# Performance work log

Measured on AMD Instinct MI355X. Metric: run time of the kernel, lower is better.

Reference implementation:

```python
import jax, jax.numpy as jnp
import numpy as np

B, T, TR, DIM, H = 1, 4096, 1024, 1536, 12
DH = DIM // H          # 128
EPS = 1e-6             # RMSNorm eps
REF_SCALE = 1.0


def setup_inputs() -> dict:
    key = jax.random.key(0)
    ks = jax.random.split(key, 20)
    s = 0.02
    w = lambda k: jax.random.normal(k, (DIM, DIM), jnp.float32) * s
    b = lambda k: jax.random.normal(k, (DIM,), jnp.float32) * 0.01
    theta = jax.random.uniform(ks[2], (T, DH // 2), jnp.float32) * (2.0 * np.pi)
    return {
        "hidden_states": jax.random.normal(ks[0], (B, T, DIM), jnp.float32),
        "ref_hidden_states": jax.random.normal(ks[1], (B, TR, DIM), jnp.float32),
        "rot_cos": jnp.cos(theta),
        "rot_sin": jnp.sin(theta),
        "Wq": w(ks[3]), "bq": b(ks[4]),
        "Wk": w(ks[5]), "bk": b(ks[6]),
        "Wv": w(ks[7]), "bv": b(ks[8]),
        "Wkr": w(ks[9]), "bkr": b(ks[10]),
        "Wvr": w(ks[11]), "bvr": b(ks[12]),
        "Wo": w(ks[13]), "bo": b(ks[14]),
        "gq": jnp.ones((DIM,), jnp.float32),
        "gk": jnp.ones((DIM,), jnp.float32),
    }


def _rmsnorm(x, g):
    return x * jax.lax.rsqrt(jnp.mean(x * x, axis=-1, keepdims=True) + EPS) * g


def _heads(x):  # [B, T, DIM] -> [B, H, T, DH]
    return x.reshape(B, -1, H, DH).transpose(0, 2, 1, 3)


def _merge(x):  # [B, H, T, DH] -> [B, T, DIM]
    return x.transpose(0, 2, 1, 3).reshape(B, -1, DIM)


def _rope(x, c, s):
    # consecutive pairs along DH form complex numbers (view_as_complex semantics)
    xe, xo = x[..., 0::2], x[..., 1::2]
    c = c[None, None]  # [1,1,T,DH/2]
    s = s[None, None]
    re = xe * c - xo * s
    im = xe * s + xo * c
    return jnp.stack([re, im], axis=-1).reshape(x.shape)


def _attn(q, k, v):
    scale = 1.0 / jnp.sqrt(jnp.asarray(DH, q.dtype))
    p = jax.nn.softmax(jnp.einsum("bhqd,bhkd->bhqk", q, k) * scale, axis=-1)
    return jnp.einsum("bhqk,bhkd->bhqd", p, v)


def reference(hidden_states, ref_hidden_states, rot_cos, rot_sin,
              Wq, bq, Wk, bk, Wv, bv, Wkr, bkr, Wvr, bvr, Wo, bo, gq, gk):
    # QKV projections (self-attention: encoder_hidden_states = hidden_states)
    q_lin = hidden_states @ Wq + bq
    k_lin = hidden_states @ Wk + bk
    v_lin = hidden_states @ Wv + bv

    # ---- reference-attention branch (uses pre-RoPE query) ----
    ref_q = _heads(_rmsnorm(q_lin, gq))
    ref_k = _heads(_rmsnorm(ref_hidden_states @ Wkr + bkr, gk))
    ref_v = _heads(ref_hidden_states @ Wvr + bvr)
    ref_out = _merge(_attn(ref_q, ref_k, ref_v))  # [B, T, DIM]

    # ---- main attention with QK-norm + RoPE ----
    q = _rope(_heads(_rmsnorm(q_lin, gq)), rot_cos, rot_sin)
    k = _rope(_heads(_rmsnorm(k_lin, gk)), rot_cos, rot_sin)
    v = _heads(v_lin)
    main_out = _merge(_attn(q, k, v))  # [B, T, DIM]

    # scaled residual combine + output projection (dropout = identity)
    out = main_out + REF_SCALE * ref_out
    return out @ Wo + bo
```

## Files before the change

### kernel.cpp

```cpp
#include <hip/hip_runtime.h>

typedef unsigned short u16;
typedef unsigned int u32;
typedef __attribute__((ext_vector_type(8))) short short8;
typedef __attribute__((ext_vector_type(4))) float f32x4;

__device__ inline u16 f2b(float f) {
  u32 u = __builtin_bit_cast(u32, f);
  u += 0x7fff + ((u >> 16) & 1);
  return (u16)(u >> 16);
}
__device__ inline float b2f(u16 u) {
  return __builtin_bit_cast(float, (u32)u << 16);
}
__device__ inline u32 pack_bf16_rn(float a, float b) {
  const u32 ua = __builtin_bit_cast(u32, a) + 0x8000u;
  const u32 ub = __builtin_bit_cast(u32, b) + 0x8000u;
  return (ua >> 16) | (ub & 0xffff0000u);
}
__device__ inline void c_store(float* p, float v) { *p = v; }
__device__ inline void c_store(u16* p, float v) { *p = f2b(v); }

__device__ inline float fexp2(float x) {
#if __has_builtin(__builtin_amdgcn_exp2f)
  return __builtin_amdgcn_exp2f(x);
#else
  return exp2f(x);
#endif
}

typedef const __attribute__((address_space(1))) u32 gu32;
typedef __attribute__((address_space(3))) u32 lu32;
__device__ inline void async16(const u16* g, u16* l) {
  __builtin_amdgcn_global_load_lds((gu32*)g, (lu32*)l, 16, 0, 0);
}

#define QS (0.08838834764831843f * 1.4426950408889634f)

template <int MI, typename TC>
__global__ __launch_bounds__(256) void gemm128_kernel(
    const u16* __restrict__ A, long lda,
    const u16* __restrict__ Bt, long ldb,
    TC* __restrict__ C0, TC* __restrict__ C1, TC* __restrict__ C2, long ldc,
    const float* b0, const float* b1, const float* b2,
    int K) {
  __shared__ u16 As[32 * MI * 32];
  __shared__ u16 Bs[128 * 32];

  const int tid = threadIdx.x;
  const int lane = tid & 63;
  const int w = tid >> 6;
  const int r = lane & 15;
  const int quad = lane >> 4;
  const int m0 = blockIdx.y * (32 * MI);
  const int nb = blockIdx.x * 128;
  const int seg = nb / 1536;
  const int nc = nb - seg * 1536;
  TC* C = seg == 0 ? C0 : (seg == 1 ? C1 : C2);
  const float* bias = seg == 0 ? b0 : (seg == 1 ? b1 : b2);

  const int srow = lane >> 2;
  const int sx = ((lane & 3) ^ (srow & 3)) * 8;
  const u16* Ag = A + (size_t)(m0 + w * 8 * MI + srow) * lda + sx;
  const u16* Bg = Bt + (size_t)(nb + w * 32 + srow) * ldb + sx;
  u16* Al[MI / 2];
#pragma unroll
  for (int j = 0; j < MI / 2; ++j) Al[j] = &As[(w * 8 * MI + 16 * j) * 32];
  u16* const Bl0 = &Bs[(w * 32) * 32];
  u16* const Bl1 = &Bs[(w * 32 + 16) * 32];

  const int wm = (w >> 1) * (16 * MI);
  const int wn = (w & 1) * 64;

  f32x4 acc[MI][4];
#pragma unroll
  for (int i = 0; i < MI; ++i)
#pragma unroll
    for (int j = 0; j < 4; ++j) acc[i][j] = (f32x4){0.f, 0.f, 0.f, 0.f};

  const int fco = (quad ^ (r & 3)) * 8;

  for (int kk = 0; kk < K; kk += 32) {
    __syncthreads();
#pragma unroll
    for (int j = 0; j < MI / 2; ++j) async16(Ag + kk + (size_t)(16 * j) * lda, Al[j]);
    async16(Bg + kk, Bl0);
    async16(Bg + kk + 16 * ldb, Bl1);
    __syncthreads();

    short8 af[MI], bf[4];
#pragma unroll
    for (int mi = 0; mi < MI; ++mi)
      af[mi] = *reinterpret_cast<const short8*>(&As[(wm + 16 * mi + r) * 32 + fco]);
#pragma unroll
    for (int ni = 0; ni < 4; ++ni)
      bf[ni] = *reinterpret_cast<const short8*>(&Bs[(wn + 16 * ni + r) * 32 + fco]);
#pragma unroll
    for (int mi = 0; mi < MI; ++mi)
#pragma unroll
      for (int ni = 0; ni < 4; ++ni)
        acc[mi][ni] = __builtin_amdgcn_mfma_f32_16x16x32_bf16(af[mi], bf[ni], acc[mi][ni], 0, 0, 0);
  }

#pragma unroll
  for (int mi = 0; mi < MI; ++mi)
#pragma unroll
    for (int ni = 0; ni < 4; ++ni)
#pragma unroll
      for (int rr = 0; rr < 4; ++rr) {
        const int row = m0 + wm + 16 * mi + 4 * quad + rr;
        const int col = nc + wn + 16 * ni + r;
        c_store(&C[(size_t)row * ldc + col], acc[mi][ni][rr] + bias[col]);
      }
}

__global__ __launch_bounds__(256) void conv2_kernel(
    const float* __restrict__ xa, u16* __restrict__ ya, int n8a,
    const float* __restrict__ xb, u16* __restrict__ yb, int n8b) {
  int i = blockIdx.x * 256 + threadIdx.x;
  const float* x;
  u16* y;
  if (i < n8a) {
    x = xa; y = ya;
  } else {
    i -= n8a;
    if (i >= n8b) return;
    x = xb; y = yb;
  }
  const float4 v0 = reinterpret_cast<const float4*>(x)[2 * i];
  const float4 v1 = reinterpret_cast<const float4*>(x)[2 * i + 1];
  uint4 rv;
  rv.x = (u32)f2b(v0.x) | ((u32)f2b(v0.y) << 16);
  rv.y = (u32)f2b(v0.z) | ((u32)f2b(v0.w) << 16);
  rv.z = (u32)f2b(v1.x) | ((u32)f2b(v1.y) << 16);
  rv.w = (u32)f2b(v1.z) | ((u32)f2b(v1.w) << 16);
  reinterpret_cast<uint4*>(y)[i] = rv;
}

__device__ inline void transconv_body(const float* __restrict__ W, u16* __restrict__ Wt) {
  __shared__ u16 Ls[64 * 72];
  const int tid = threadIdx.x;
  const int k0 = blockIdx.y * 64;
  const int n0 = blockIdx.x * 64;
#pragma unroll
  for (int i = 0; i < 4; ++i) {
    const int c = tid + 256 * i;
    const int row = c >> 4;
    const int c4 = (c & 15) * 4;
    const float4 v = *reinterpret_cast<const float4*>(&W[(size_t)(k0 + row) * 1536 + n0 + c4]);
    Ls[(c4 + 0) * 72 + row] = f2b(v.x);
    Ls[(c4 + 1) * 72 + row] = f2b(v.y);
    Ls[(c4 + 2) * 72 + row] = f2b(v.z);
    Ls[(c4 + 3) * 72 + row] = f2b(v.w);
  }
  __syncthreads();
#pragma unroll
  for (int i = 0; i < 2; ++i) {
    const int c = tid + 256 * i;
    const int n = c >> 3;
    const int kc = (c & 7) * 8;
    u16 tmp[8];
#pragma unroll
    for (int j = 0; j < 8; ++j) tmp[j] = Ls[n * 72 + kc + j];
    *reinterpret_cast<uint4*>(&Wt[(size_t)(n0 + n) * 1536 + k0 + kc]) =
        *reinterpret_cast<const uint4*>(tmp);
  }
}

__global__ __launch_bounds__(256) void transconv6_kernel(
    const float* W0, const float* W1, const float* W2,
    const float* W3, const float* W4, const float* W5,
    u16* T0, u16* T1, u16* T2, u16* T3, u16* T4, u16* T5) {
  const int z = blockIdx.z;
  const float* W = z == 0 ? W0 : z == 1 ? W1 : z == 2 ? W2 : z == 3 ? W3 : z == 4 ? W4 : W5;
  u16* Wt = z == 0 ? T0 : z == 1 ? T1 : z == 2 ? T2 : z == 3 ? T3 : z == 4 ? T4 : T5;
  transconv_body(W, Wt);
}

__global__ __launch_bounds__(256) void rmsnorm3_kernel(
    const u16* xq, const u16* xk, const u16* xkr,
    const float* gq, const float* gk,
    const float* rc, const float* rs,
    u16* oq_plain, u16* oq_rope, u16* ok_rope, u16* okr_plain) {
  __shared__ float red[4];
  const int z = blockIdx.y;
  const int row = blockIdx.x;
  if (z == 2 && row >= 1024) return;
  const u16* x; const float* g; u16* po; u16* pr; float sc;
  if (z == 0)      { x = xq;  g = gq; po = oq_plain; pr = oq_rope; sc = QS;  }
  else if (z == 1) { x = xk;  g = gk; po = nullptr;  pr = ok_rope; sc = 1.f; }
  else             { x = xkr; g = gk; po = okr_plain; pr = nullptr; sc = 1.f; }

  const int tid = threadIdx.x;
  const u32* xr = reinterpret_cast<const u32*>(x + (size_t)row * 1536);
  float xe[3], xo[3];
  float ss = 0.f;
#pragma unroll
  for (int j = 0; j < 3; ++j) {
    const u32 u = xr[tid + 256 * j];
    const float e = b2f((u16)(u & 0xffff));
    const float o = b2f((u16)(u >> 16));
    xe[j] = e; xo[j] = o;
    ss += e * e + o * o;
  }
#pragma unroll
  for (int off = 32; off; off >>= 1) ss += __shfl_xor(ss, off, 64);
  if ((tid & 63) == 0) red[tid >> 6] = ss;
  __syncthreads();
  const float total = red[0] + red[1] + red[2] + red[3];
  const float rinv = rsqrtf(total * (1.0f / 1536.0f) + 1e-6f) * sc;
  u32* po32 = po ? reinterpret_cast<u32*>(po + (size_t)row * 1536) : nullptr;
  u32* pr32 = pr ? reinterpret_cast<u32*>(pr + (size_t)row * 1536) : nullptr;
#pragma unroll
  for (int j = 0; j < 3; ++j) {
    const int p = tid + 256 * j;
    const float2 gg = reinterpret_cast<const float2*>(g)[p];
    const float e = xe[j] * rinv * gg.x;
    const float o = xo[j] * rinv * gg.y;
    if (po32) po32[p] = (u32)f2b(e) | ((u32)f2b(o) << 16);
    if (pr32) {
      const int i = p & 63;
      const float c = rc[row * 64 + i];
      const float s = rs[row * 64 + i];
      const float re = e * c - o * s;
      const float im = e * s + o * c;
      pr32[p] = (u32)f2b(re) | ((u32)f2b(im) << 16);
    }
  }
}

__global__ __launch_bounds__(256) void vtrans2_kernel(
    const u16* __restrict__ V0, u16* __restrict__ Vt0,
    const u16* __restrict__ V1, u16* __restrict__ Vt1) {
  __shared__ u16 Ls[64 * 136];
  const int z = blockIdx.z;
  const int kvLen = z == 0 ? 4096 : 1024;
  const int kv0 = blockIdx.x * 64;
  if (kv0 >= kvLen) return;
  const u16* V = z == 0 ? V0 : V1;
  u16* Vt = z == 0 ? Vt0 : Vt1;
  const int tid = threadIdx.x;
  const int h = blockIdx.y;
#pragma unroll
  for (int i = 0; i < 4; ++i) {
    const int c = tid + 256 * i;
    const int row = c >> 4, c8 = c & 15;
    *reinterpret_cast<uint4*>(&Ls[row * 136 + 8 * c8]) =
        *reinterpret_cast<const uint4*>(V + (size_t)(kv0 + row) * 1536 + h * 128 + 8 * c8);
  }
  __syncthreads();
#pragma unroll
  for (int i = 0; i < 4; ++i) {
    const int c = tid + 256 * i;
    const int d = c >> 3, kc = c & 7;
    u16 tmp[8];
#pragma unroll
    for (int j = 0; j < 8; ++j) tmp[j] = Ls[(8 * kc + j) * 136 + d];
    *reinterpret_cast<uint4*>(Vt + ((size_t)h * 128 + d) * kvLen + kv0 + 8 * kc) =
        *reinterpret_cast<const uint4*>(tmp);
  }
}

__global__ __launch_bounds__(256, 4) void flash_kernel(
    const u16* __restrict__ Q, const u16* __restrict__ K,
    const u16* __restrict__ Vt, float* __restrict__ O,
    u16* __restrict__ Ob, int kvLen, int addO) {
  __shared__ u16 Ks[2][32 * 128];
  __shared__ u16 Vs[2][128 * 32];
  __shared__ u16 Pb[4][16 * 40];
  __shared__ float ab[4][16];

  const int tid = threadIdx.x;
  const int lane = tid & 63;
  const int w = tid >> 6;
  const int r = lane & 15;
  const int quad = lane >> 4;
  const int h = blockIdx.y;
  const int q0 = blockIdx.x * 64;
  const int qrow = q0 + 16 * w + r;
  const int s3 = r & 3;

  short8 qf[4];
  {
    const u16* qbase = Q + (size_t)qrow * 1536 + h * 128 + 8 * quad;
#pragma unroll
    for (int ks = 0; ks < 4; ++ks)
      qf[ks] = *reinterpret_cast<const short8*>(qbase + 32 * ks);
  }

  const u16* Kb = K + h * 128;
  const u16* Vb = Vt + (size_t)h * 128 * kvLen;
  u32 koff[2], voff[2];
  int klo[2], vlo[2];
  {
    const int p16 = lane & 15, rin = lane >> 4;
    const int p4 = lane & 3, din = lane >> 2;
#pragma unroll
    for (int j = 0; j < 2; ++j) {
      const int row = 8 * w + 4 * j + rin;
      koff[j] = (u32)row * 1536u + 8u * (u32)(p16 ^ (row & 15));
      klo[j] = (8 * w + 4 * j) * 128;
      const int d = 32 * w + 16 * j + din;
      voff[j] = (u32)d * (u32)kvLen + 8u * (u32)(p4 ^ (d & 3));
      vlo[j] = (32 * w + 16 * j) * 32;
    }
  }

  f32x4 Oc[8];
#pragma unroll
  for (int dt = 0; dt < 8; ++dt) Oc[dt] = (f32x4){0.f, 0.f, 0.f, 0.f};
  float m_i = -1e30f, l_i = 0.f;

  const int nt = kvLen >> 5;

  {
    const size_t ko0 = 0, vo0 = 0;
#pragma unroll
    for (int j = 0; j < 2; ++j) async16(Kb + ko0 + koff[j], &Ks[0][klo[j]]);
#pragma unroll
    for (int j = 0; j < 2; ++j) async16(Vb + vo0 + voff[j], &Vs[0][vlo[j]]);
  }

  for (int t = 0; t < nt; ++t) {
    const int buf = t & 1;
    __syncthreads();
    if (t + 1 < nt) {
      const size_t ko = (size_t)(t + 1) * (32 * 1536);
      const size_t vo = (size_t)(t + 1) * 32;
#pragma unroll
      for (int j = 0; j < 2; ++j) async16(Kb + ko + koff[j], &Ks[buf ^ 1][klo[j]]);
#pragma unroll
      for (int j = 0; j < 2; ++j) async16(Vb + vo + voff[j], &Vs[buf ^ 1][vlo[j]]);
    }

    f32x4 St[2];
#pragma unroll
    for (int mt = 0; mt < 2; ++mt) St[mt] = (f32x4){0.f, 0.f, 0.f, 0.f};
    __builtin_amdgcn_s_setprio(1);
#pragma unroll
    for (int mt = 0; mt < 2; ++mt) {
      const u16* kp = &Ks[buf][(16 * mt + r) * 128];
#pragma unroll
      for (int ks = 0; ks < 4; ++ks) {
        const short8 af = *reinterpret_cast<const short8*>(kp + 8 * ((quad + 4 * ks) ^ r));
        St[mt] = __builtin_amdgcn_mfma_f32_16x16x32_bf16(af, qf[ks], St[mt], 0, 0, 0);
      }
    }
    __builtin_amdgcn_s_setprio(0);

    float mloc = -1e30f;
#pragma unroll
    for (int mt = 0; mt < 2; ++mt)
#pragma unroll
      for (int rr = 0; rr < 4; ++rr) mloc = fmaxf(mloc, St[mt][rr]);
    mloc = fmaxf(mloc, __shfl_xor(mloc, 16, 64));
    mloc = fmaxf(mloc, __shfl_xor(mloc, 32, 64));

    float alpha = 1.0f;
    if (__any(mloc > m_i + 11.5f)) {
      const float mn = fmaxf(m_i, mloc);
      alpha = fexp2(m_i - mn);
      m_i = mn;
      if (quad == 0) ab[w][r] = alpha;
      const float4 a4 = *reinterpret_cast<const float4*>(&ab[w][4 * quad]);
#pragma unroll
      for (int dt = 0; dt < 8; ++dt) {
        Oc[dt][0] *= a4.x; Oc[dt][1] *= a4.y; Oc[dt][2] *= a4.z; Oc[dt][3] *= a4.w;
      }
    }

    float psum = 0.f;
    uint2 pk[2];
#pragma unroll
    for (int mt = 0; mt < 2; ++mt) {
      const float p0 = fexp2(St[mt][0] - m_i);
      const float p1 = fexp2(St[mt][1] - m_i);
      const float p2 = fexp2(St[mt][2] - m_i);
      const float p3 = fexp2(St[mt][3] - m_i);
      psum += (p0 + p1) + (p2 + p3);
      pk[mt].x = pack_bf16_rn(p0, p1);
      pk[mt].y = pack_bf16_rn(p2, p3);
    }
    psum += __shfl_xor(psum, 16, 64);
    psum += __shfl_xor(psum, 32, 64);
    l_i = l_i * alpha + psum;

#pragma unroll
    for (int mt = 0; mt < 2; ++mt)
      *reinterpret_cast<uint2*>(&Pb[w][r * 40 + 16 * mt + 4 * quad]) = pk[mt];
    {
      const short8 pa = *reinterpret_cast<const short8*>(&Pb[w][r * 40 + 8 * quad]);
      __builtin_amdgcn_s_setprio(1);
#pragma unroll
      for (int dt = 0; dt < 8; ++dt) {
        const int d = 16 * dt + r;
        const short8 b0 = *reinterpret_cast<const short8*>(&Vs[buf][d * 32 + 8 * (quad ^ s3)]);
        Oc[dt] = __builtin_amdgcn_mfma_f32_16x16x32_bf16(pa, b0, Oc[dt], 0, 0, 0);
      }
      __builtin_amdgcn_s_setprio(0);
    }
  }

  if (quad == 0) ab[w][r] = 1.0f / l_i;
  const float4 li4 = *reinterpret_cast<const float4*>(&ab[w][4 * quad]);
  const float lv[4] = {li4.x, li4.y, li4.z, li4.w};
  float* obf = O + (size_t)(q0 + 16 * w) * 1536 + h * 128;
  u16* obb = Ob + (size_t)(q0 + 16 * w) * 1536 + h * 128;
#pragma unroll
  for (int rr = 0; rr < 4; ++rr) {
    float* orow = obf + (size_t)(4 * quad + rr) * 1536 + r;
    u16* brow = obb + (size_t)(4 * quad + rr) * 1536 + r;
#pragma unroll
    for (int dt = 0; dt < 8; ++dt) {
      float v = Oc[dt][rr] * lv[rr];
      if (addO) {
        v += orow[16 * dt];
        brow[16 * dt] = f2b(v);
      } else {
        orow[16 * dt] = v;
      }
    }
  }
}

extern "C" void kernel_launch(void* const* d_in, const int* in_sizes, int n_in,
                              void* d_out, int out_size, void* d_ws, size_t ws_size,
                              hipStream_t stream) {
  (void)in_sizes; (void)n_in; (void)out_size; (void)ws_size;
  constexpr int T = 4096, TR = 1024, DIM = 1536, NH = 12;

  const float* hs  = (const float*)d_in[0];
  const float* rhs = (const float*)d_in[1];
  const float* rc  = (const float*)d_in[2];
  const float* rs  = (const float*)d_in[3];
  const float* Wq  = (const float*)d_in[4];
  const float* bq  = (const float*)d_in[5];
  const float* Wk  = (const float*)d_in[6];
  const float* bk  = (const float*)d_in[7];
  const float* Wv  = (const float*)d_in[8];
  const float* bv  = (const float*)d_in[9];
  const float* Wkr = (const float*)d_in[10];
  const float* bkr = (const float*)d_in[11];
  const float* Wvr = (const float*)d_in[12];
  const float* bvr = (const float*)d_in[13];
  const float* Wo  = (const float*)d_in[14];
  const float* bo  = (const float*)d_in[15];
  const float* gq  = (const float*)d_in[16];
  const float* gk  = (const float*)d_in[17];
  float* out = (float*)d_out;

  char* ws = (char*)d_ws;
  size_t off = 0;
  auto alloc = [&](size_t bytes) -> void* {
    void* p = ws + off;
    off += (bytes + 255) & ~(size_t)255;
    return p;
  };
  u16* bQ    = (u16*)alloc((size_t)T * DIM * 2);
  u16* bQr   = (u16*)alloc((size_t)T * DIM * 2);
  u16* bK    = (u16*)alloc((size_t)T * DIM * 2);
  u16* bV    = (u16*)alloc((size_t)T * DIM * 2);
  u16* bKr   = (u16*)alloc((size_t)TR * DIM * 2);
  u16* bVr   = (u16*)alloc((size_t)TR * DIM * 2);
  float* bO  = (float*)alloc((size_t)T * DIM * 4);
  u16* bHs   = (u16*)alloc((size_t)T * DIM * 2);
  u16* bRhs  = (u16*)alloc((size_t)TR * DIM * 2);
  u16* bWqkv = (u16*)alloc((size_t)3 * DIM * DIM * 2);
  u16* bWr   = (u16*)alloc((size_t)2 * DIM * DIM * 2);
  u16* bWoT  = (u16*)alloc((size_t)DIM * DIM * 2);
  u16* VtG = bHs;
  u16* VtR = bRhs;
  u16* bOb = bWqkv;

  const dim3 blk(256);

  conv2_kernel<<<dim3((T * DIM / 8 + TR * DIM / 8 + 255) / 256), blk, 0, stream>>>(
      hs, bHs, T * DIM / 8, rhs, bRhs, TR * DIM / 8);

  transconv6_kernel<<<dim3(24, 24, 6), blk, 0, stream>>>(
      Wq, Wk, Wv, Wkr, Wvr, Wo,
      bWqkv + 0 * (size_t)DIM * DIM, bWqkv + 1 * (size_t)DIM * DIM,
      bWqkv + 2 * (size_t)DIM * DIM, bWr + 0 * (size_t)DIM * DIM,
      bWr + 1 * (size_t)DIM * DIM, bWoT);

  gemm128_kernel<4, u16><<<dim3(36, 32), blk, 0, stream>>>(
      bHs, DIM, bWqkv, DIM, bQ, bK, bV, DIM, bq, bk, bv, DIM);
  gemm128_kernel<2, u16><<<dim3(24, 16), blk, 0, stream>>>(
      bRhs, DIM, bWr, DIM, bKr, bVr, (u16*)nullptr, DIM, bkr, bvr, nullptr, DIM);

  rmsnorm3_kernel<<<dim3(T, 3), blk, 0, stream>>>(
      bQ, bK, bKr, gq, gk, rc, rs, bQ, bQr, bK, bKr);

  vtrans2_kernel<<<dim3(T / 64, NH, 2), blk, 0, stream>>>(bV, VtG, bVr, VtR);

  flash_kernel<<<dim3(T / 64, NH), blk, 0, stream>>>(bQ, bKr, VtR, bO, bOb, TR, 0);
  flash_kernel<<<dim3(T / 64, NH), blk, 0, stream>>>(bQr, bK, VtG, bO, bOb, T, 1);

  gemm128_kernel<2, float><<<dim3(12, 64), blk, 0, stream>>>(
      bOb, DIM, bWoT, DIM, out, (float*)nullptr, (float*)nullptr, DIM, bo, nullptr, nullptr, DIM);
}
```

Before: 564.1 us.

## Fuse reference and main flash attention passes into one kernel

The two flash-attention launches (reference branch, then main branch) become one kernel that runs both passes per block, keeps the reference output in registers and sums the two in-register before writing the bf16 result. This drops the fp32 intermediate output buffer, its write and read-back, and one launch. The V-tile LDS swizzle also changes from r&3 to (r>>1)&3, in both the load offset and the read index. In exchange, each block holds eight more accumulator vectors, which raises register pressure under the 4-blocks-per-SM launch bound.

```diff
diff --git a/kernel.cpp b/kernel.cpp
--- a/kernel.cpp
+++ b/kernel.cpp
@@ -262,9 +262,11 @@
 }
 
 __global__ __launch_bounds__(256, 4) void flash_kernel(
-    const u16* __restrict__ Q, const u16* __restrict__ K,
-    const u16* __restrict__ Vt, float* __restrict__ O,
-    u16* __restrict__ Ob, int kvLen, int addO) {
+    const u16* __restrict__ Qc, const u16* __restrict__ Kc,
+    const u16* __restrict__ Vc, int kvLenC,
+    const u16* __restrict__ Qm, const u16* __restrict__ Km,
+    const u16* __restrict__ Vm, int kvLenM,
+    u16* __restrict__ Ob) {
   __shared__ u16 Ks[2][32 * 128];
   __shared__ u16 Vs[2][128 * 32];
   __shared__ u16 Pb[4][16 * 40];
@@ -278,148 +280,148 @@
   const int h = blockIdx.y;
   const int q0 = blockIdx.x * 64;
   const int qrow = q0 + 16 * w + r;
-  const int s3 = r & 3;
-
-  short8 qf[4];
-  {
-    const u16* qbase = Q + (size_t)qrow * 1536 + h * 128 + 8 * quad;
-#pragma unroll
-    for (int ks = 0; ks < 4; ++ks)
-      qf[ks] = *reinterpret_cast<const short8*>(qbase + 32 * ks);
-  }
-
-  const u16* Kb = K + h * 128;
-  const u16* Vb = Vt + (size_t)h * 128 * kvLen;
-  u32 koff[2], voff[2];
-  int klo[2], vlo[2];
-  {
-    const int p16 = lane & 15, rin = lane >> 4;
-    const int p4 = lane & 3, din = lane >> 2;
-#pragma unroll
-    for (int j = 0; j < 2; ++j) {
-      const int row = 8 * w + 4 * j + rin;
-      koff[j] = (u32)row * 1536u + 8u * (u32)(p16 ^ (row & 15));
-      klo[j] = (8 * w + 4 * j) * 128;
-      const int d = 32 * w + 16 * j + din;
-      voff[j] = (u32)d * (u32)kvLen + 8u * (u32)(p4 ^ (d & 3));
-      vlo[j] = (32 * w + 16 * j) * 32;
+  const int fv = (r >> 1) & 3;
+
+  auto run_pass = [&](const u16* __restrict__ Q, const u16* __restrict__ K,
+                      const u16* __restrict__ Vt, int kvLen, f32x4* Oc) {
+    short8 qf[4];
+    {
+      const u16* qbase = Q + (size_t)qrow * 1536 + h * 128 + 8 * quad;
+#pragma unroll
+      for (int ks = 0; ks < 4; ++ks)
+        qf[ks] = *reinterpret_cast<const short8*>(qbase + 32 * ks);
     }
-  }
-
+
+    const u16* Kb = K + h * 128;
+    const u16* Vb = Vt + (size_t)h * 128 * kvLen;
+    u32 koff[2], voff[2];
+    int klo[2], vlo[2];
+    {
+      const int p16 = lane & 15, rin = lane >> 4;
+      const int p4 = lane & 3, din = lane >> 2;
+#pragma unroll
+      for (int j = 0; j < 2; ++j) {
+        const int row = 8 * w + 4 * j + rin;
+        koff[j] = (u32)row * 1536u + 8u * (u32)(p16 ^ (row & 15));
+        klo[j] = (8 * w + 4 * j) * 128;
+        const int d = 32 * w + 16 * j + din;
+        voff[j] = (u32)d * (u32)kvLen + 8u * (u32)(p4 ^ ((din >> 1) & 3));
+        vlo[j] = (32 * w + 16 * j) * 32;
+      }
+    }
+
+#pragma unroll
+    for (int dt = 0; dt < 8; ++dt) Oc[dt] = (f32x4){0.f, 0.f, 0.f, 0.f};
+    float m_i = -1e30f, l_i = 0.f;
+
+    const int nt = kvLen >> 5;
+
+#pragma unroll
+    for (int j = 0; j < 2; ++j) async16(Kb + koff[j], &Ks[0][klo[j]]);
+#pragma unroll
+    for (int j = 0; j < 2; ++j) async16(Vb + voff[j], &Vs[0][vlo[j]]);
+
+    for (int t = 0; t < nt; ++t) {
+      const int buf = t & 1;
+      __syncthreads();
+      if (t + 1 < nt) {
+        const size_t ko = (size_t)(t + 1) * (32 * 1536);
+        const size_t vo = (size_t)(t + 1) * 32;
+#pragma unroll
+        for (int j = 0; j < 2; ++j) async16(Kb + ko + koff[j], &Ks[buf ^ 1][klo[j]]);
+#pragma unroll
+        for (int j = 0; j < 2; ++j) async16(Vb + vo + voff[j], &Vs[buf ^ 1][vlo[j]]);
+      }
+
+      f32x4 St[2];
+#pragma unroll
+      for (int mt = 0; mt < 2; ++mt) St[mt] = (f32x4){0.f, 0.f, 0.f, 0.f};
+      __builtin_amdgcn_s_setprio(1);
+#pragma unroll
+      for (int mt = 0; mt < 2; ++mt) {
+        const u16* kp = &Ks[buf][(16 * mt + r) * 128];
+#pragma unroll
+        for (int ks = 0; ks < 4; ++ks) {
+          const short8 af = *reinterpret_cast<const short8*>(kp + 8 * ((quad + 4 * ks) ^ r));
+          St[mt] = __builtin_amdgcn_mfma_f32_16x16x32_bf16(af, qf[ks], St[mt], 0, 0, 0);
+        }
+      }
+      __builtin_amdgcn_s_setprio(0);
+
+      float mloc = -1e30f;
+#pragma unroll
+      for (int mt = 0; mt < 2; ++mt)
+#pragma unroll
+        for (int rr = 0; rr < 4; ++rr) mloc = fmaxf(mloc, St[mt][rr]);
+      mloc = fmaxf(mloc, __shfl_xor(mloc, 16, 64));
+      mloc = fmaxf(mloc, __shfl_xor(mloc, 32, 64));
+
+      float alpha = 1.0f;
+      if (__any(mloc > m_i + 11.5f)) {
+        const float mn = fmaxf(m_i, mloc);
+        alpha = fexp2(m_i - mn);
+        m_i = mn;
+        if (quad == 0) ab[w][r] = alpha;
+        const float4 a4 = *reinterpret_cast<const float4*>(&ab[w][4 * quad]);
+#pragma unroll
+        for (int dt = 0; dt < 8; ++dt) {
+          Oc[dt][0] *= a4.x; Oc[dt][1] *= a4.y; Oc[dt][2] *= a4.z; Oc[dt][3] *= a4.w;
+        }
+      }
+
+      float psum = 0.f;
+      uint2 pk[2];
+#pragma unroll
+      for (int mt = 0; mt < 2; ++mt) {
+        const float p0 = fexp2(St[mt][0] - m_i);
+        const float p1 = fexp2(St[mt][1] - m_i);
+        const float p2 = fexp2(St[mt][2] - m_i);
+        const float p3 = fexp2(St[mt][3] - m_i);
+        psum += (p0 + p1) + (p2 + p3);
+        pk[mt].x = pack_bf16_rn(p0, p1);
+        pk[mt].y = pack_bf16_rn(p2, p3);
+      }
+      psum += __shfl_xor(psum, 16, 64);
+      psum += __shfl_xor(psum, 32, 64);
+      l_i = l_i * alpha + psum;
+
+#pragma unroll
+      for (int mt = 0; mt < 2; ++mt)
+        *reinterpret_cast<uint2*>(&Pb[w][r * 40 + 16 * mt + 4 * quad]) = pk[mt];
+      {
+        const short8 pa = *reinterpret_cast<const short8*>(&Pb[w][r * 40 + 8 * quad]);
+        __builtin_amdgcn_s_setprio(1);
+#pragma unroll
+        for (int dt = 0; dt < 8; ++dt) {
+          const int d = 16 * dt + r;
+          const short8 b0 = *reinterpret_cast<const short8*>(&Vs[buf][d * 32 + 8 * (quad ^ fv)]);
+          Oc[dt] = __builtin_amdgcn_mfma_f32_16x16x32_bf16(pa, b0, Oc[dt], 0, 0, 0);
+        }
+        __builtin_amdgcn_s_setprio(0);
+      }
+    }
+
+    if (quad == 0) ab[w][r] = 1.0f / l_i;
+    const float4 li4 = *reinterpret_cast<const float4*>(&ab[w][4 * quad]);
+#pragma unroll
+    for (int dt = 0; dt < 8; ++dt) {
+      Oc[dt][0] *= li4.x; Oc[dt][1] *= li4.y; Oc[dt][2] *= li4.z; Oc[dt][3] *= li4.w;
+    }
+  };
+
+  f32x4 Ocr[8];
+  run_pass(Qc, Kc, Vc, kvLenC, Ocr);
+  __syncthreads();
   f32x4 Oc[8];
-#pragma unroll
-  for (int dt = 0; dt < 8; ++dt) Oc[dt] = (f32x4){0.f, 0.f, 0.f, 0.f};
-  float m_i = -1e30f, l_i = 0.f;
-
-  const int nt = kvLen >> 5;
-
-  {
-    const size_t ko0 = 0, vo0 = 0;
-#pragma unroll
-    for (int j = 0; j < 2; ++j) async16(Kb + ko0 + koff[j], &Ks[0][klo[j]]);
-#pragma unroll
-    for (int j = 0; j < 2; ++j) async16(Vb + vo0 + voff[j], &Vs[0][vlo[j]]);
-  }
-
-  for (int t = 0; t < nt; ++t) {
-    const int buf = t & 1;
-    __syncthreads();
-    if (t + 1 < nt) {
-      const size_t ko = (size_t)(t + 1) * (32 * 1536);
-      const size_t vo = (size_t)(t + 1) * 32;
-#pragma unroll
-      for (int j = 0; j < 2; ++j) async16(Kb + ko + koff[j], &Ks[buf ^ 1][klo[j]]);
-#pragma unroll
-      for (int j = 0; j < 2; ++j) async16(Vb + vo + voff[j], &Vs[buf ^ 1][vlo[j]]);
-    }
-
-    f32x4 St[2];
-#pragma unroll
-    for (int mt = 0; mt < 2; ++mt) St[mt] = (f32x4){0.f, 0.f, 0.f, 0.f};
-    __builtin_amdgcn_s_setprio(1);
-#pragma unroll
-    for (int mt = 0; mt < 2; ++mt) {
-      const u16* kp = &Ks[buf][(16 * mt + r) * 128];
-#pragma unroll
-      for (int ks = 0; ks < 4; ++ks) {
-        const short8 af = *reinterpret_cast<const short8*>(kp + 8 * ((quad + 4 * ks) ^ r));
-        St[mt] = __builtin_amdgcn_mfma_f32_16x16x32_bf16(af, qf[ks], St[mt], 0, 0, 0);
-      }
-    }
-    __builtin_amdgcn_s_setprio(0);
-
-    float mloc = -1e30f;
-#pragma unroll
-    for (int mt = 0; mt < 2; ++mt)
-#pragma unroll
-      for (int rr = 0; rr < 4; ++rr) mloc = fmaxf(mloc, St[mt][rr]);
-    mloc = fmaxf(mloc, __shfl_xor(mloc, 16, 64));
-    mloc = fmaxf(mloc, __shfl_xor(mloc, 32, 64));
-
-    float alpha = 1.0f;
-    if (__any(mloc > m_i + 11.5f)) {
-      const float mn = fmaxf(m_i, mloc);
-      alpha = fexp2(m_i - mn);
-      m_i = mn;
-      if (quad == 0) ab[w][r] = alpha;
-      const float4 a4 = *reinterpret_cast<const float4*>(&ab[w][4 * quad]);
-#pragma unroll
-      for (int dt = 0; dt < 8; ++dt) {
-        Oc[dt][0] *= a4.x; Oc[dt][1] *= a4.y; Oc[dt][2] *= a4.z; Oc[dt][3] *= a4.w;
-      }
-    }
-
-    float psum = 0.f;
-    uint2 pk[2];
-#pragma unroll
-    for (int mt = 0; mt < 2; ++mt) {
-      const float p0 = fexp2(St[mt][0] - m_i);
-      const float p1 = fexp2(St[mt][1] - m_i);
-      const float p2 = fexp2(St[mt][2] - m_i);
-      const float p3 = fexp2(St[mt][3] - m_i);
-      psum += (p0 + p1) + (p2 + p3);
-      pk[mt].x = pack_bf16_rn(p0, p1);
-      pk[mt].y = pack_bf16_rn(p2, p3);
-    }
-    psum += __shfl_xor(psum, 16, 64);
-    psum += __shfl_xor(psum, 32, 64);
-    l_i = l_i * alpha + psum;
-
-#pragma unroll
-    for (int mt = 0; mt < 2; ++mt)
-      *reinterpret_cast<uint2*>(&Pb[w][r * 40 + 16 * mt + 4 * quad]) = pk[mt];
-    {
-      const short8 pa = *reinterpret_cast<const short8*>(&Pb[w][r * 40 + 8 * quad]);
-      __builtin_amdgcn_s_setprio(1);
-#pragma unroll
-      for (int dt = 0; dt < 8; ++dt) {
-        const int d = 16 * dt + r;
-        const short8 b0 = *reinterpret_cast<const short8*>(&Vs[buf][d * 32 + 8 * (quad ^ s3)]);
-        Oc[dt] = __builtin_amdgcn_mfma_f32_16x16x32_bf16(pa, b0, Oc[dt], 0, 0, 0);
-      }
-      __builtin_amdgcn_s_setprio(0);
-    }
-  }
-
-  if (quad == 0) ab[w][r] = 1.0f / l_i;
-  const float4 li4 = *reinterpret_cast<const float4*>(&ab[w][4 * quad]);
-  const float lv[4] = {li4.x, li4.y, li4.z, li4.w};
-  float* obf = O + (size_t)(q0 + 16 * w) * 1536 + h * 128;
+  run_pass(Qm, Km, Vm, kvLenM, Oc);
+
   u16* obb = Ob + (size_t)(q0 + 16 * w) * 1536 + h * 128;
 #pragma unroll
   for (int rr = 0; rr < 4; ++rr) {
-    float* orow = obf + (size_t)(4 * quad + rr) * 1536 + r;
     u16* brow = obb + (size_t)(4 * quad + rr) * 1536 + r;
 #pragma unroll
-    for (int dt = 0; dt < 8; ++dt) {
-      float v = Oc[dt][rr] * lv[rr];
-      if (addO) {
-        v += orow[16 * dt];
-        brow[16 * dt] = f2b(v);
-      } else {
-        orow[16 * dt] = v;
-      }
-    }
+    for (int dt = 0; dt < 8; ++dt)
+      brow[16 * dt] = f2b(Oc[dt][rr] + Ocr[dt][rr]);
   }
 }
 
@@ -462,7 +464,6 @@
   u16* bV    = (u16*)alloc((size_t)T * DIM * 2);
   u16* bKr   = (u16*)alloc((size_t)TR * DIM * 2);
   u16* bVr   = (u16*)alloc((size_t)TR * DIM * 2);
-  float* bO  = (float*)alloc((size_t)T * DIM * 4);
   u16* bHs   = (u16*)alloc((size_t)T * DIM * 2);
   u16* bRhs  = (u16*)alloc((size_t)TR * DIM * 2);
   u16* bWqkv = (u16*)alloc((size_t)3 * DIM * DIM * 2);
@@ -493,8 +494,8 @@
 
   vtrans2_kernel<<<dim3(T / 64, NH, 2), blk, 0, stream>>>(bV, VtG, bVr, VtR);
 
-  flash_kernel<<<dim3(T / 64, NH), blk, 0, stream>>>(bQ, bKr, VtR, bO, bOb, TR, 0);
-  flash_kernel<<<dim3(T / 64, NH), blk, 0, stream>>>(bQr, bK, VtG, bO, bOb, T, 1);
+  flash_kernel<<<dim3(T / 64, NH), blk, 0, stream>>>(
+      bQ, bKr, VtR, TR, bQr, bK, VtG, T, bOb);
 
   gemm128_kernel<2, float><<<dim3(12, 64), blk, 0, stream>>>(
       bOb, DIM, bWoT, DIM, out, (float*)nullptr, (float*)nullptr, DIM, bo, nullptr, nullptr, DIM);
```

Result: faster. 542.6 us (-3.8%).
